# Kernel tuning notes

Hardware: AMD Instinct MI355X
Metric: run time of the kernel (lower is better)

Reference implementation:

```python
import jax, jax.numpy as jnp
import numpy as np

N, E, G = 50000, 1000000, 128          # nodes, edges, graphs
NODE_DIM, EDGE_DIM, HID, EMB = 8, 3, 32, 64


def setup_inputs() -> dict:
    key = jax.random.key(0)
    ks = list(jax.random.split(key, 16))
    def nrm(k, shape, s=1.0):
        return jax.random.normal(k, shape, dtype=jnp.float32) * s
    return {
        "x": nrm(ks[0], (N, NODE_DIM)),
        "edge_attr": nrm(ks[1], (E, EDGE_DIM)),
        "the_ratios": jax.random.uniform(ks[2], (5,), dtype=jnp.float32),
        "edge_index": jax.random.randint(ks[3], (2, E), 0, N),
        "batch": jnp.sort(jax.random.randint(ks[4], (N,), 0, G)),
        "the_ids": jax.random.randint(ks[5], (5,), 0, 118),
        # edge_nn: Linear(3,32) -> ReLU -> Linear(32, 8*32)
        "W1": nrm(ks[6], (EDGE_DIM, 32), 0.3), "b1": jnp.zeros((32,), jnp.float32),
        "W2": nrm(ks[7], (32, NODE_DIM * HID), 0.1), "b2": jnp.zeros((NODE_DIM * HID,), jnp.float32),
        "emb": nrm(ks[8], (118, EMB), 0.1),
        # NNConv root weight + bias
        "root": nrm(ks[9], (NODE_DIM, HID), 0.3), "conv_bias": jnp.zeros((HID,), jnp.float32),
        "fc0_w": nrm(ks[10], (HID + EMB, 64), 0.1), "fc0_b": jnp.zeros((64,), jnp.float32),
        "fc1_w": nrm(ks[11], (64, 32), 0.1), "fc1_b": jnp.zeros((32,), jnp.float32),
        "fc2_w": nrm(ks[12], (32, 1), 0.1), "fc2_b": jnp.zeros((1,), jnp.float32),
    }


def reference(x, edge_attr, the_ratios, edge_index, batch, the_ids,
              W1, b1, W2, b2, emb, root, conv_bias,
              fc0_w, fc0_b, fc1_w, fc1_b, fc2_w, fc2_b):
    src, dst = edge_index[0], edge_index[1]
    # per-edge weight matrix from edge MLP: [E, NODE_DIM, HID]
    h = jax.nn.relu(edge_attr @ W1 + b1)
    We = (h @ W2 + b2).reshape(E, NODE_DIM, HID)
    # gather source node feats, per-edge matmul: [E, HID]
    msg = jnp.einsum('ei,eio->eo', x[src], We)
    # scatter-mean to target nodes
    s = jax.ops.segment_sum(msg, dst, num_segments=N)
    cnt = jax.ops.segment_sum(jnp.ones((E,), msg.dtype), dst, num_segments=N)
    agg = s / jnp.maximum(cnt, 1.0)[:, None]
    # NNConv root transform + bias, then ReLU
    h_node = jax.nn.relu(x @ root + agg + conv_bias)
    # global mean pool over graphs
    gs = jax.ops.segment_sum(h_node, batch, num_segments=G)
    gc = jax.ops.segment_sum(jnp.ones((N,), h_node.dtype), batch, num_segments=G)
    pooled = gs / jnp.maximum(gc, 1.0)[:, None]
    # weighted element embedding, broadcast to all graphs
    u = jnp.sum(emb[the_ids] * the_ratios[:, None], axis=0)
    z = jnp.concatenate([pooled, jnp.broadcast_to(u, (G, EMB))], axis=1)
    z = jax.nn.relu(z @ fc0_w + fc0_b)
    z = jax.nn.relu(z @ fc1_w + fc1_b)
    return z @ fc2_w + fc2_b
```

## Files before the change

### kernel.cpp

```cpp
#include <hip/hip_runtime.h>

#define NODE_DIM 8

typedef __attribute__((ext_vector_type(8))) short short8;
typedef __attribute__((ext_vector_type(4))) float f32x4;

#define DOT8(xv, WT) ((xv)[0]*(WT)[0] + (xv)[1]*(WT)[1] + (xv)[2]*(WT)[2] + (xv)[3]*(WT)[3] + \
                      (xv)[4]*(WT)[4] + (xv)[5]*(WT)[5] + (xv)[6]*(WT)[6] + (xv)[7]*(WT)[7])

static __device__ __forceinline__ unsigned cvt_pk_bf16(float a, float b) {
    unsigned r;
    asm("v_cvt_pk_bf16_f32 %0, %1, %2" : "=v"(r) : "v"(a), "v"(b));
    return r;
}


static __device__ __forceinline__ void stage_b_frags(short* lds_b,
                                                     const float* __restrict__ W2,
                                                     const float* __restrict__ b2)
{
    const int t = threadIdx.x;
    for (int f = t; f < 18 * 64 * 8; f += 256) {
        const int j   = f & 7;
        const int ln  = (f >> 3) & 63;
        const int fid = f >> 9;
        const int kk  = fid >> 1, ot = fid & 1;
        const int qq  = ln >> 4, ol = ln & 15;
        float v;
        if (kk < 8) v = W2[(kk * 4 + qq) * 256 + j * 32 + ot * 16 + ol];
        else        v = (qq == 0) ? b2[j * 32 + ot * 16 + ol] : 0.f;
        unsigned uv = __float_as_uint(v);
        uv = (uv + 0x7fffu + ((uv >> 16) & 1u)) >> 16;
        lds_b[f] = (short)uv;
    }
}

static __device__ __forceinline__ void edge_compute(const short* lds_b,
                                                    const float* __restrict__ x,
                                                    const float* __restrict__ ea,
                                                    const int* __restrict__ eidx,
                                                    const float* __restrict__ W1,
                                                    const float* __restrict__ b1,
                                                    float* __restrict__ s,
                                                    int* __restrict__ cnt,
                                                    int E)
{
    const int t    = threadIdx.x;
    const int lane = t & 63;
    const int e_l  = lane & 15;
    const int q    = lane >> 4;

    float w10[8], w11[8], w12[8], b1r[8];
#pragma unroll
    for (int t2 = 0; t2 < 8; ++t2) {
        const int k = 4 * t2 + q;
        w10[t2] = W1[k]; w11[t2] = W1[32 + k]; w12[t2] = W1[64 + k]; b1r[t2] = b1[k];
    }

    const int wave = blockIdx.x * 4 + (t >> 6);
    const int nwav = gridDim.x * 4;
    const int ngrp = (E + 15) / 16;

    for (int g0 = 2 * wave; g0 < ngrp; g0 += 2 * nwav) {
        const bool v1    = (g0 + 1) < ngrp;
        const int  base0 = g0 * 16;
        const int  base1 = (v1 ? g0 + 1 : g0) * 16;

        int ej0 = base0 + e_l; if (ej0 >= E) ej0 = E - 1;
        int ej1 = base1 + e_l; if (ej1 >= E) ej1 = E - 1;

        const int src0 = eidx[ej0];
        const int dst0 = eidx[E + ej0];
        const int src1 = eidx[ej1];
        const int dst1 = eidx[E + ej1];
        const float ea00 = ea[3 * ej0], ea01 = ea[3 * ej0 + 1], ea02 = ea[3 * ej0 + 2];
        const float ea10 = ea[3 * ej1], ea11 = ea[3 * ej1 + 1], ea12 = ea[3 * ej1 + 2];
        const float4 xa0 = *(const float4*)(x + (size_t)(unsigned)src0 * 8);
        const float4 xb0 = *(const float4*)(x + (size_t)(unsigned)src0 * 8 + 4);
        const float4 xa1 = *(const float4*)(x + (size_t)(unsigned)src1 * 8);
        const float4 xb1 = *(const float4*)(x + (size_t)(unsigned)src1 * 8 + 4);
        const float xr0[8] = {xa0.x, xa0.y, xa0.z, xa0.w, xb0.x, xb0.y, xb0.z, xb0.w};
        const float xr1[8] = {xa1.x, xa1.y, xa1.z, xa1.w, xb1.x, xb1.y, xb1.z, xb1.w};

        float h0[8], h1[8];
#pragma unroll
        for (int t2 = 0; t2 < 8; ++t2) {
            const float z0 = b1r[t2] + ea00 * w10[t2] + ea01 * w11[t2] + ea02 * w12[t2];
            const float z1 = b1r[t2] + ea10 * w10[t2] + ea11 * w11[t2] + ea12 * w12[t2];
            h0[t2] = z0 > 0.f ? z0 : 0.f;
            h1[t2] = z1 > 0.f ? z1 : 0.f;
        }

        f32x4 a00 = {0.f, 0.f, 0.f, 0.f};
        f32x4 a01 = {0.f, 0.f, 0.f, 0.f};
        f32x4 a10 = {0.f, 0.f, 0.f, 0.f};
        f32x4 a11 = {0.f, 0.f, 0.f, 0.f};

        {
            union { short8 v; unsigned u[4]; } id0, id1;
#pragma unroll
            for (int p = 0; p < 4; ++p) {
                id0.u[p] = cvt_pk_bf16(xr0[2 * p], xr0[2 * p + 1]);
                id1.u[p] = cvt_pk_bf16(xr1[2 * p], xr1[2 * p + 1]);
            }
            const short8 bf0 = *(const short8*)&lds_b[(16 * 64 + lane) * 8];
            const short8 bf1 = *(const short8*)&lds_b[(17 * 64 + lane) * 8];
            a00 = __builtin_amdgcn_mfma_f32_16x16x32_bf16(id0.v, bf0, a00, 0, 0, 0);
            a01 = __builtin_amdgcn_mfma_f32_16x16x32_bf16(id0.v, bf1, a01, 0, 0, 0);
            a10 = __builtin_amdgcn_mfma_f32_16x16x32_bf16(id1.v, bf0, a10, 0, 0, 0);
            a11 = __builtin_amdgcn_mfma_f32_16x16x32_bf16(id1.v, bf1, a11, 0, 0, 0);
        }

#pragma unroll
        for (int kk = 0; kk < 8; ++kk) {
            const short8 bf0 = *(const short8*)&lds_b[((kk * 2 + 0) * 64 + lane) * 8];
            const short8 bf1 = *(const short8*)&lds_b[((kk * 2 + 1) * 64 + lane) * 8];
            const float hk0 = h0[kk], hk1 = h1[kk];
            union { short8 v; unsigned u[4]; } af0, af1;
#pragma unroll
            for (int p = 0; p < 4; ++p) {
                af0.u[p] = cvt_pk_bf16(hk0 * xr0[2 * p], hk0 * xr0[2 * p + 1]);
                af1.u[p] = cvt_pk_bf16(hk1 * xr1[2 * p], hk1 * xr1[2 * p + 1]);
            }
            a00 = __builtin_amdgcn_mfma_f32_16x16x32_bf16(af0.v, bf0, a00, 0, 0, 0);
            a01 = __builtin_amdgcn_mfma_f32_16x16x32_bf16(af0.v, bf1, a01, 0, 0, 0);
            a10 = __builtin_amdgcn_mfma_f32_16x16x32_bf16(af1.v, bf0, a10, 0, 0, 0);
            a11 = __builtin_amdgcn_mfma_f32_16x16x32_bf16(af1.v, bf1, a11, 0, 0, 0);
        }

#pragma unroll
        for (int r = 0; r < 4; ++r) {
            const int m   = q * 4 + r;
            const int dr0 = __shfl(dst0, m, 16);
            const int dr1 = __shfl(dst1, m, 16);
            if (base0 + m < E) {
                atomicAdd(&s[(size_t)(unsigned)dr0 * 32 + e_l],      a00[r]);
                atomicAdd(&s[(size_t)(unsigned)dr0 * 32 + 16 + e_l], a01[r]);
            }
            if (v1 && base1 + m < E) {
                atomicAdd(&s[(size_t)(unsigned)dr1 * 32 + e_l],      a10[r]);
                atomicAdd(&s[(size_t)(unsigned)dr1 * 32 + 16 + e_l], a11[r]);
            }
        }
        if (lane < 16) {
            if (base0 + e_l < E)       atomicAdd(&cnt[dst0], 1);
            if (v1 && base1 + e_l < E) atomicAdd(&cnt[dst1], 1);
        }
    }
}

__global__ __launch_bounds__(256, 4)
void edge_kernel(const float* __restrict__ x,
                 const float* __restrict__ ea,
                 const int* __restrict__ eidx,
                 const float* __restrict__ W1, const float* __restrict__ b1,
                 const float* __restrict__ W2, const float* __restrict__ b2,
                 float* __restrict__ s, int* __restrict__ cnt, int E)
{
    __shared__ __align__(16) short lds_b[18 * 64 * 8];
    stage_b_frags(lds_b, W2, b2);
    __syncthreads();
    edge_compute(lds_b, x, ea, eidx, W1, b1, s, cnt, E);
}

__global__ __launch_bounds__(256)
void node_mlp_kernel(const float* __restrict__ s,
                     const int* __restrict__ cnt,
                     const float* __restrict__ x,
                     const float* __restrict__ root,
                     const float* __restrict__ conv_bias,
                     const int* __restrict__ batch,
                     const float* __restrict__ ratios,
                     const int* __restrict__ ids,
                     const float* __restrict__ emb,
                     const float* __restrict__ fc0w, const float* __restrict__ fc0b,
                     const float* __restrict__ fc1w, const float* __restrict__ fc1b,
                     const float* __restrict__ fc2w, const float* __restrict__ fc2b,
                     float* __restrict__ out, int N)
{
    __shared__ float red[256];
    __shared__ float zs[96];
    __shared__ float z1[64];
    __shared__ float z2[32];
    __shared__ int   seg[2];

    const int g    = blockIdx.x;
    const int t    = threadIdx.x;
    const int o    = t & 31;
    const int slot = t >> 5;

    if (t < 2) {
        const int target = g + t;
        int lo = 0, hi = N;
        while (lo < hi) {
            const int mid = (lo + hi) >> 1;
            if (batch[mid] < target) lo = mid + 1; else hi = mid;
        }
        seg[t] = lo;
    }
    __syncthreads();
    const int s0 = seg[0], s1 = seg[1];

    float rootr[8];
#pragma unroll
    for (int i = 0; i < 8; ++i) rootr[i] = root[i * 32 + o];
    const float cb = conv_bias[o];

    float acc = 0.f;
    for (int n = s0 + slot; n < s1; n += 8) {
        const int   c    = cnt[n];
        const float rinv = 1.f / (float)(c > 1 ? c : 1);
        const float* xp  = x + (size_t)n * 8;
        float xv[8];
#pragma unroll
        for (int i = 0; i < 8; ++i) xv[i] = xp[i];
        const float t2 = s[(size_t)n * 32 + o] * rinv + cb + DOT8(xv, rootr);
        acc += t2 > 0.f ? t2 : 0.f;
    }
    red[t] = acc;
    __syncthreads();

    if (t < 32) {
        float p = 0.f;
#pragma unroll
        for (int c2 = 0; c2 < 8; ++c2) p += red[t + 32 * c2];
        float c = (float)(s1 - s0);
        if (c < 1.f) c = 1.f;
        zs[t] = p / c;
    }
    if (t >= 32 && t < 96) {
        const int j = t - 32;
        float u = 0.f;
#pragma unroll
        for (int r = 0; r < 5; ++r) u += ratios[r] * emb[(size_t)ids[r] * 64 + j];
        zs[32 + j] = u;
    }
    __syncthreads();

    if (t < 64) {
        float a = fc0b[t];
        for (int k = 0; k < 96; ++k) a += zs[k] * fc0w[k * 64 + t];
        z1[t] = a > 0.f ? a : 0.f;
    }
    __syncthreads();

    if (t < 32) {
        float a = fc1b[t];
        for (int k = 0; k < 64; ++k) a += z1[k] * fc1w[k * 32 + t];
        z2[t] = a > 0.f ? a : 0.f;
    }
    __syncthreads();

    if (t == 0) {
        float a = fc2b[0];
        for (int k = 0; k < 32; ++k) a += z2[k] * fc2w[k];
        out[g] = a;
    }
}

extern "C" void kernel_launch(void* const* d_in, const int* in_sizes, int n_in,
                              void* d_out, int out_size, void* d_ws, size_t ws_size,
                              hipStream_t stream)
{
    const float* x         = (const float*)d_in[0];
    const float* ea        = (const float*)d_in[1];
    const float* ratios    = (const float*)d_in[2];
    const int*   eidx      = (const int*)  d_in[3];
    const int*   batch     = (const int*)  d_in[4];
    const int*   ids       = (const int*)  d_in[5];
    const float* W1        = (const float*)d_in[6];
    const float* b1        = (const float*)d_in[7];
    const float* W2        = (const float*)d_in[8];
    const float* b2        = (const float*)d_in[9];
    const float* emb       = (const float*)d_in[10];
    const float* root      = (const float*)d_in[11];
    const float* conv_bias = (const float*)d_in[12];
    const float* fc0w      = (const float*)d_in[13];
    const float* fc0b      = (const float*)d_in[14];
    const float* fc1w      = (const float*)d_in[15];
    const float* fc1b      = (const float*)d_in[16];
    const float* fc2w      = (const float*)d_in[17];
    const float* fc2b      = (const float*)d_in[18];

    const int N = in_sizes[0] / NODE_DIM;
    const int E = in_sizes[1] / 3;
    const int G = out_size;

    float* s   = (float*)d_ws;
    int*   cnt = (int*)((char*)d_ws + (size_t)N * 32 * 4);

    (void)hipMemsetAsync(d_ws, 0, (size_t)N * 32 * 4 + (size_t)N * 4, stream);

    edge_kernel<<<2048, 256, 0, stream>>>(x, ea, eidx, W1, b1, W2, b2, s, cnt, E);
    node_mlp_kernel<<<G, 256, 0, stream>>>(s, cnt, x, root, conv_bias, batch,
                                           ratios, ids, emb,
                                           fc0w, fc0b, fc1w, fc1b, fc2w, fc2b,
                                           (float*)d_out, N);
}
```

Measured before the change: 278.2 us.

## Pack scatter sums as biased fixed-point pairs in 64-bit integer atomics

Each message value is converted to a biased 32-bit fixed-point integer (scale 2^15, bias 2^21). Neighbouring lanes' values are then combined with a shuffle and packed into a single 64-bit integer atomicAdd. The goal is to halve the number of global atomics in the scatter phase and to use integer atomics instead of float atomics. The node kernel decodes the sum by subtracting count times the bias. This risks losing precision through quantisation and overflowing or carrying between the packed fields if partial sums grow large.

```diff
diff --git a/kernel.cpp b/kernel.cpp
--- a/kernel.cpp
+++ b/kernel.cpp
@@ -14,6 +14,13 @@
     return r;
 }
 
+
+#define FIX_SCALE 32768.0f
+#define FIX_BIAS  (1u << 21)
+
+static __device__ __forceinline__ unsigned fix_enc(float v) {
+    return (unsigned)((int)rintf(v * FIX_SCALE) + (int)FIX_BIAS);
+}
 
 static __device__ __forceinline__ void stage_b_frags(short* lds_b,
                                                      const float* __restrict__ W2,
@@ -41,7 +48,7 @@
                                                     const int* __restrict__ eidx,
                                                     const float* __restrict__ W1,
                                                     const float* __restrict__ b1,
-                                                    float* __restrict__ s,
+                                                    unsigned long long* __restrict__ s,
                                                     int* __restrict__ cnt,
                                                     int E)
 {
@@ -60,6 +67,9 @@
     const int wave = blockIdx.x * 4 + (t >> 6);
     const int nwav = gridDim.x * 4;
     const int ngrp = (E + 15) / 16;
+
+    const bool ev = (e_l & 1) == 0;
+    const int  qw = ev ? (e_l >> 1) : (8 + (e_l >> 1));
 
     for (int g0 = 2 * wave; g0 < ngrp; g0 += 2 * nwav) {
         const bool v1    = (g0 + 1) < ngrp;
@@ -133,14 +143,23 @@
             const int m   = q * 4 + r;
             const int dr0 = __shfl(dst0, m, 16);
             const int dr1 = __shfl(dst1, m, 16);
-            if (base0 + m < E) {
-                atomicAdd(&s[(size_t)(unsigned)dr0 * 32 + e_l],      a00[r]);
-                atomicAdd(&s[(size_t)(unsigned)dr0 * 32 + 16 + e_l], a01[r]);
-            }
-            if (v1 && base1 + m < E) {
-                atomicAdd(&s[(size_t)(unsigned)dr1 * 32 + e_l],      a10[r]);
-                atomicAdd(&s[(size_t)(unsigned)dr1 * 32 + 16 + e_l], a11[r]);
-            }
+            const float p00 = __shfl_xor(a00[r], 1);
+            const float p01 = __shfl_xor(a01[r], 1);
+            const float p10 = __shfl_xor(a10[r], 1);
+            const float p11 = __shfl_xor(a11[r], 1);
+            unsigned lo0, hi0, lo1, hi1;
+            if (ev) { lo0 = fix_enc(a00[r]); hi0 = fix_enc(p00);
+                      lo1 = fix_enc(a10[r]); hi1 = fix_enc(p10); }
+            else    { lo0 = fix_enc(p01);    hi0 = fix_enc(a01[r]);
+                      lo1 = fix_enc(p11);    hi1 = fix_enc(a11[r]); }
+            const unsigned long long val0 = (unsigned long long)lo0 |
+                                            ((unsigned long long)hi0 << 32);
+            const unsigned long long val1 = (unsigned long long)lo1 |
+                                            ((unsigned long long)hi1 << 32);
+            if (base0 + m < E)
+                atomicAdd(&s[(size_t)(unsigned)dr0 * 16 + qw], val0);
+            if (v1 && base1 + m < E)
+                atomicAdd(&s[(size_t)(unsigned)dr1 * 16 + qw], val1);
         }
         if (lane < 16) {
             if (base0 + e_l < E)       atomicAdd(&cnt[dst0], 1);
@@ -155,7 +174,7 @@
                  const int* __restrict__ eidx,
                  const float* __restrict__ W1, const float* __restrict__ b1,
                  const float* __restrict__ W2, const float* __restrict__ b2,
-                 float* __restrict__ s, int* __restrict__ cnt, int E)
+                 unsigned long long* __restrict__ s, int* __restrict__ cnt, int E)
 {
     __shared__ __align__(16) short lds_b[18 * 64 * 8];
     stage_b_frags(lds_b, W2, b2);
@@ -164,7 +183,7 @@
 }
 
 __global__ __launch_bounds__(256)
-void node_mlp_kernel(const float* __restrict__ s,
+void node_mlp_kernel(const unsigned long long* __restrict__ s,
                      const int* __restrict__ cnt,
                      const float* __restrict__ x,
                      const float* __restrict__ root,
@@ -189,6 +208,9 @@
     const int o    = t & 31;
     const int slot = t >> 5;
 
+    const int qw  = (o < 16) ? (o >> 1) : (8 + ((o - 16) >> 1));
+    const int fld = o & 1;
+
     if (t < 2) {
         const int target = g + t;
         int lo = 0, hi = N;
@@ -210,11 +232,14 @@
     for (int n = s0 + slot; n < s1; n += 8) {
         const int   c    = cnt[n];
         const float rinv = 1.f / (float)(c > 1 ? c : 1);
+        const unsigned long long w = s[(size_t)n * 16 + qw];
+        const unsigned fr  = fld ? (unsigned)(w >> 32) : (unsigned)w;
+        const float    sv  = (float)((int)(fr - (unsigned)c * FIX_BIAS)) / FIX_SCALE;
         const float* xp  = x + (size_t)n * 8;
         float xv[8];
 #pragma unroll
         for (int i = 0; i < 8; ++i) xv[i] = xp[i];
-        const float t2 = s[(size_t)n * 32 + o] * rinv + cb + DOT8(xv, rootr);
+        const float t2 = sv * rinv + cb + DOT8(xv, rootr);
         acc += t2 > 0.f ? t2 : 0.f;
     }
     red[t] = acc;
@@ -286,10 +311,10 @@
     const int E = in_sizes[1] / 3;
     const int G = out_size;
 
-    float* s   = (float*)d_ws;
-    int*   cnt = (int*)((char*)d_ws + (size_t)N * 32 * 4);
-
-    (void)hipMemsetAsync(d_ws, 0, (size_t)N * 32 * 4 + (size_t)N * 4, stream);
+    unsigned long long* s = (unsigned long long*)d_ws;
+    int* cnt = (int*)((char*)d_ws + (size_t)N * 16 * 8);
+
+    (void)hipMemsetAsync(d_ws, 0, (size_t)N * 16 * 8 + (size_t)N * 4, stream);
 
     edge_kernel<<<2048, 256, 0, stream>>>(x, ea, eidx, W1, b1, W2, b2, s, cnt, E);
     node_mlp_kernel<<<G, 256, 0, stream>>>(s, cnt, x, root, conv_bias, batch,
```

After: 276.4 us. Within noise of the previous version (-0.6%).
